# Performance work log

Measured on AMD Instinct MI355X. Metric: run time of the kernel, lower is better.

## Reference

```python
import math
import jax, jax.numpy as jnp
import numpy as np

L, D, DFF, V, TCTX, H = 6, 1024, 4096, 32000, 1024, 16
B, T = 2, 1024


def _ln(x, w, b, eps=1e-5):
    mu = jnp.mean(x, axis=-1, keepdims=True)
    var = jnp.var(x, axis=-1, keepdims=True)
    return (x - mu) * jax.lax.rsqrt(var + eps) * w + b


def setup_inputs() -> dict:
    key = jax.random.key(0)
    ks = jax.random.split(key, 8)
    s = 0.02
    s_res = 0.02 / math.sqrt(2 * L)  # out_proj / ffn.2 init
    tok_emb = jax.random.normal(ks[0], (V, D), jnp.float32) * s
    pos_emb = jax.random.normal(ks[1], (TCTX, D), jnp.float32) * s
    qkv_w = jax.random.normal(ks[2], (L, 3 * D, D), jnp.float32) * s
    out_w = jax.random.normal(ks[3], (L, D, D), jnp.float32) * s_res
    ffn1_w = jax.random.normal(ks[4], (L, DFF, D), jnp.float32) * s
    ffn2_w = jax.random.normal(ks[5], (L, D, DFF), jnp.float32) * s_res
    ln1_w = jnp.ones((L, D), jnp.float32); ln1_b = jnp.zeros((L, D), jnp.float32)
    ln2_w = jnp.ones((L, D), jnp.float32); ln2_b = jnp.zeros((L, D), jnp.float32)
    lnf_w = jnp.ones((D,), jnp.float32);  lnf_b = jnp.zeros((D,), jnp.float32)
    idx = jax.random.randint(ks[6], (B, T), 0, V, dtype=jnp.int32)
    return dict(idx=idx, tok_emb=tok_emb, pos_emb=pos_emb,
                ln1_w=ln1_w, ln1_b=ln1_b, qkv_w=qkv_w, out_w=out_w,
                ln2_w=ln2_w, ln2_b=ln2_b, ffn1_w=ffn1_w, ffn2_w=ffn2_w,
                lnf_w=lnf_w, lnf_b=lnf_b)


def reference(idx, tok_emb, pos_emb, ln1_w, ln1_b, qkv_w, out_w,
              ln2_w, ln2_b, ffn1_w, ffn2_w, lnf_w, lnf_b):
    b, t = idx.shape
    d = tok_emb.shape[1]
    hd = d // H
    scale = 1.0 / math.sqrt(hd)
    causal = jnp.tril(jnp.ones((t, t), bool))  # [T,T]

    x = tok_emb[idx] + pos_emb[:t][None]  # [B,T,D]
    n_layers = qkv_w.shape[0]
    for l in range(n_layers):
        # attention
        h = _ln(x, ln1_w[l], ln1_b[l])
        qkv = h @ qkv_w[l].T  # [B,T,3D]
        q, k, v = jnp.split(qkv, 3, axis=-1)
        q = q.reshape(b, t, H, hd); k = k.reshape(b, t, H, hd); v = v.reshape(b, t, H, hd)
        scores = jnp.einsum('bqhd,bkhd->bhqk', q, k) * scale
        scores = jnp.where(causal[None, None], scores, -jnp.inf)
        attn = jax.nn.softmax(scores, axis=-1)
        o = jnp.einsum('bhqk,bkhd->bqhd', attn, v).reshape(b, t, d)
        x = x + o @ out_w[l].T
        # FFN
        h = _ln(x, ln2_w[l], ln2_b[l])
        x = x + jax.nn.gelu(h @ ffn1_w[l].T, approximate=False) @ ffn2_w[l].T
    x = _ln(x, lnf_w, lnf_b)
    logits = x @ tok_emb.T  # tied lm_head, [B,T,V]
    return logits
```

## Files before the change

### kernel.cpp

```cpp
#include <hip/hip_runtime.h>
#include <math.h>

typedef unsigned short u16;
typedef short short8 __attribute__((ext_vector_type(8)));
typedef float floatx4 __attribute__((ext_vector_type(4)));
typedef u16 u16x4 __attribute__((ext_vector_type(4)));

#define L_ 6
#define D_ 1024
#define DFF_ 4096
#define V_ 32000
#define T_ 1024
#define B_ 2
#define H_ 16
#define M_ (B_*T_)

__device__ __forceinline__ float b2f(u16 v){ union{unsigned u; float f;} x; x.u = ((unsigned)v)<<16; return x.f; }
__device__ __forceinline__ u16 f2bf(float f){ union{float f; unsigned u;} x; x.f=f; unsigned r = x.u + 0x7fffu + ((x.u>>16)&1u); return (u16)(r>>16); }

__device__ __forceinline__ void gload16(const u16* g, u16* l){
  __builtin_amdgcn_global_load_lds((const __attribute__((address_space(1))) void*)g,
                                   (__attribute__((address_space(3))) void*)l, 16, 0, 0);
}

__global__ __launch_bounds__(256) void embed_kernel(const int* __restrict__ idx,
    const float* __restrict__ tok, const float* __restrict__ pos, float* __restrict__ x)
{
  int m = blockIdx.x;
  int t = m & (T_-1);
  int id = idx[m];
  int d = threadIdx.x*4;
  floatx4 tv = *(const floatx4*)(tok + (size_t)id*D_ + d);
  floatx4 pv = *(const floatx4*)(pos + (size_t)t*D_ + d);
  floatx4 r = tv + pv;
  *(floatx4*)(x + (size_t)m*D_ + d) = r;
}

__global__ __launch_bounds__(256) void cvt_kernel(const float* __restrict__ src, u16* __restrict__ dst)
{
  size_t i = ((size_t)blockIdx.x*256 + threadIdx.x)*8;
  floatx4 a = *(const floatx4*)(src + i);
  floatx4 b = *(const floatx4*)(src + i + 4);
  short8 o;
  #pragma unroll
  for (int j=0;j<4;j++){ o[j] = (short)f2bf(a[j]); o[4+j] = (short)f2bf(b[j]); }
  *(short8*)(dst + i) = o;
}

__global__ __launch_bounds__(256) void ln_kernel(const float* __restrict__ x,
    const float* __restrict__ w, const float* __restrict__ b, u16* __restrict__ out)
{
  int row = blockIdx.x, tid = threadIdx.x;
  const float* xr = x + (size_t)row*D_;
  floatx4 v = *(const floatx4*)(xr + tid*4);
  float s  = v[0]+v[1]+v[2]+v[3];
  float sq = v[0]*v[0]+v[1]*v[1]+v[2]*v[2]+v[3]*v[3];
  #pragma unroll
  for (int m=32;m>0;m>>=1){ s += __shfl_xor(s,m); sq += __shfl_xor(sq,m); }
  __shared__ float red[8];
  if ((tid&63)==0){ red[tid>>6]=s; red[4+(tid>>6)]=sq; }
  __syncthreads();
  float st  = red[0]+red[1]+red[2]+red[3];
  float sqt = red[4]+red[5]+red[6]+red[7];
  float mu = st*(1.0f/D_);
  float rs = rsqrtf(sqt*(1.0f/D_) - mu*mu + 1e-5f);
  floatx4 wv = *(const floatx4*)(w + tid*4);
  floatx4 bv = *(const floatx4*)(b + tid*4);
  u16x4 o;
  #pragma unroll
  for(int j=0;j<4;j++) o[j] = f2bf((v[j]-mu)*rs*wv[j] + bv[j]);
  *(u16x4*)(out + (size_t)row*D_ + tid*4) = o;
}

#define BM 128
#define BN 128
#define BK 32

__global__ __launch_bounds__(256) void gemm_bf16(const u16* __restrict__ A,
    const u16* __restrict__ Bw, void* __restrict__ Cp,
    int M, int N, int K, int mode, int gy)
{
  __shared__ __align__(16) u16 As[2*BM*BK];
  __shared__ __align__(16) u16 Bs[2*BN*BK];
  int tid = threadIdx.x;

  int bid = blockIdx.x, nwg = gridDim.x;
  int xcd = bid & 7, o8 = bid >> 3;
  int q = nwg >> 3, r = nwg & 7;
  int wg = (xcd < r ? xcd*(q+1) : r*(q+1) + (xcd-r)*q) + o8;
  int n0 = (wg / gy) * BN;
  int m0 = (wg % gy) * BM;

  int w = tid>>6, lane = tid&63, quad = lane>>4, r16 = lane&15;
  int wm = (w>>1)*64, wn = (w&1)*64;

  int c0 = w*128 + lane;
  int c1 = c0 + 64;
  const u16* ga0 = A  + (size_t)(m0 + (c0>>2))*K + (c0&3)*8;
  const u16* ga1 = A  + (size_t)(m0 + (c1>>2))*K + (c1&3)*8;
  const u16* gb0 = Bw + (size_t)(n0 + (c0>>2))*K + (c0&3)*8;
  const u16* gb1 = Bw + (size_t)(n0 + (c1>>2))*K + (c1&3)*8;

  floatx4 acc[4][4];
  #pragma unroll
  for(int i=0;i<4;i++)
    #pragma unroll
    for(int j=0;j<4;j++) acc[i][j] = (floatx4)0.0f;

  int nt = K/BK;
  gload16(ga0, As + w*1024);
  gload16(ga1, As + w*1024 + 512);
  gload16(gb0, Bs + w*1024);
  gload16(gb1, Bs + w*1024 + 512);
  __syncthreads();

  int cur = 0;
  for (int t=0; t<nt; ++t){
    if (t+1 < nt){
      int kn = (t+1)*BK;
      int nb = (cur^1)*(BM*BK);
      gload16(ga0 + kn, As + nb + w*1024);
      gload16(ga1 + kn, As + nb + w*1024 + 512);
      gload16(gb0 + kn, Bs + nb + w*1024);
      gload16(gb1 + kn, Bs + nb + w*1024 + 512);
    }
    const u16* Ab = As + cur*(BM*BK);
    const u16* Bb = Bs + cur*(BN*BK);
    short8 af[4], bfr[4];
    #pragma unroll
    for (int i=0;i<4;i++){
      af[i]  = *(const short8*)(Ab + (wm + i*16 + r16)*BK + quad*8);
      bfr[i] = *(const short8*)(Bb + (wn + i*16 + r16)*BK + quad*8);
    }
    #pragma unroll
    for (int mi=0;mi<4;mi++)
      #pragma unroll
      for (int ni=0;ni<4;ni++)
        acc[mi][ni] = __builtin_amdgcn_mfma_f32_16x16x32_bf16(af[mi], bfr[ni], acc[mi][ni], 0,0,0);
    __syncthreads();
    cur ^= 1;
  }

  #pragma unroll
  for (int mi=0;mi<4;mi++){
    #pragma unroll
    for (int ni=0;ni<4;ni++){
      #pragma unroll
      for (int r2=0;r2<4;r2++){
        int m = m0 + wm + mi*16 + quad*4 + r2;
        int n = n0 + wn + ni*16 + r16;
        float v = acc[mi][ni][r2];
        size_t off = (size_t)m*N + n;
        if (mode==1)      ((float*)Cp)[off] = v;
        else if (mode==2) ((u16*)Cp)[off]   = f2bf(0.5f*v*(1.0f + erff(v*0.70710678118654752f)));
        else if (mode==4) ((u16*)Cp)[off]   = f2bf(v);
        else              ((float*)Cp)[off] += v;
      }
    }
  }
}

__global__ __launch_bounds__(256) void vtrans_kernel(const u16* __restrict__ qkv, u16* __restrict__ Vt)
{
  __shared__ u16 Lt[64*72];
  int bh = blockIdx.x, b = bh>>4, h = bh&15;
  int tt = blockIdx.y;
  int tid = threadIdx.x;
  #pragma unroll
  for (int cc=0; cc<2; cc++){
    int c = tid + cc*256;
    int t = c>>3, dc = (c&7)*8;
    short8 v = *(const short8*)(qkv + ((size_t)(b*T_) + tt*64 + t)*3072 + 2048 + h*64 + dc);
    *(short8*)(Lt + t*72 + dc) = v;
  }
  __syncthreads();
  #pragma unroll
  for (int cc=0; cc<2; cc++){
    int c = tid + cc*256;
    int d = c>>3, tc = (c&7)*8;
    short8 o;
    #pragma unroll
    for (int j=0;j<8;j++) o[j] = (short)Lt[(tc+j)*72 + d];
    *(short8*)(Vt + ((size_t)bh*64 + d)*T_ + tt*64 + tc) = o;
  }
}

__global__ __launch_bounds__(256) void attn_mfma(const u16* __restrict__ qkv,
    const u16* __restrict__ Vt, u16* __restrict__ out)
{
  __shared__ __align__(16) u16 Qs[64*72];
  __shared__ __align__(16) u16 Ksh[64*72];
  __shared__ __align__(16) u16 Vts[64*72];
  __shared__ __align__(16) u16 Pls[4][16*72];
  int bh = blockIdx.x, b = bh>>4, h = bh&15;
  int y = blockIdx.y;
  int qt = (y<8) ? y : 23-y;
  int tid = threadIdx.x, w = tid>>6, lane = tid&63, quad = lane>>4, r16 = lane&15;

  #pragma unroll
  for (int cc=0; cc<2; cc++){
    int c = tid + cc*256;
    int r = c>>3, dc = (c&7)*8;
    short8 v = *(const short8*)(qkv + ((size_t)(b*T_) + qt*64 + r)*3072 + h*64 + dc);
    *(short8*)(Qs + r*72 + dc) = v;
  }
  __syncthreads();
  short8 qf[2];
  qf[0] = *(const short8*)(Qs + (w*16 + r16)*72 + quad*8);
  qf[1] = *(const short8*)(Qs + (w*16 + r16)*72 + quad*8 + 32);

  floatx4 oacc[4];
  #pragma unroll
  for (int i=0;i<4;i++) oacc[i] = (floatx4)0.0f;
  float m_run[4], l_run[4];
  #pragma unroll
  for (int r=0;r<4;r++){ m_run[r] = -INFINITY; l_run[r] = 0.f; }
  int qg = qt*64 + w*16 + quad*4;

  for (int kb=0; kb<=qt; kb++){
    __syncthreads();
    #pragma unroll
    for (int cc=0; cc<2; cc++){
      int c = tid + cc*256;
      int r = c>>3, dc = (c&7)*8;
      short8 kv = *(const short8*)(qkv + ((size_t)(b*T_) + kb*64 + r)*3072 + D_ + h*64 + dc);
      *(short8*)(Ksh + r*72 + dc) = kv;
      short8 vv = *(const short8*)(Vt + ((size_t)bh*64 + r)*T_ + kb*64 + dc);
      *(short8*)(Vts + r*72 + dc) = vv;
    }
    __syncthreads();

    floatx4 sa[4];
    #pragma unroll
    for (int nt=0;nt<4;nt++) sa[nt] = (floatx4)0.0f;
    #pragma unroll
    for (int nt=0;nt<4;nt++){
      short8 kf0 = *(const short8*)(Ksh + (nt*16 + r16)*72 + quad*8);
      short8 kf1 = *(const short8*)(Ksh + (nt*16 + r16)*72 + quad*8 + 32);
      sa[nt] = __builtin_amdgcn_mfma_f32_16x16x32_bf16(qf[0], kf0, sa[nt], 0,0,0);
      sa[nt] = __builtin_amdgcn_mfma_f32_16x16x32_bf16(qf[1], kf1, sa[nt], 0,0,0);
    }
    bool diag = (kb==qt);
    #pragma unroll
    for (int nt=0;nt<4;nt++)
      #pragma unroll
      for (int r=0;r<4;r++){
        float s = sa[nt][r]*0.125f;
        if (diag && (kb*64 + nt*16 + r16) > (qg + r)) s = -INFINITY;
        sa[nt][r] = s;
      }

    float mt[4];
    #pragma unroll
    for (int r=0;r<4;r++) mt[r] = fmaxf(fmaxf(sa[0][r],sa[1][r]), fmaxf(sa[2][r],sa[3][r]));
    #pragma unroll
    for (int msk=1; msk<16; msk<<=1)
      #pragma unroll
      for (int r=0;r<4;r++) mt[r] = fmaxf(mt[r], __shfl_xor(mt[r], msk));
    float alpha[4];
    #pragma unroll
    for (int r=0;r<4;r++){
      float nm = fmaxf(m_run[r], mt[r]);
      alpha[r] = __expf(m_run[r]-nm);
      m_run[r] = nm;
    }
    float psum[4] = {0.f,0.f,0.f,0.f};
    #pragma unroll
    for (int nt=0;nt<4;nt++)
      #pragma unroll
      for (int r=0;r<4;r++){
        float p = __expf(sa[nt][r]-m_run[r]);
        sa[nt][r] = p;
        psum[r] += p;
      }
    #pragma unroll
    for (int msk=1; msk<16; msk<<=1)
      #pragma unroll
      for (int r=0;r<4;r++) psum[r] += __shfl_xor(psum[r], msk);
    #pragma unroll
    for (int r=0;r<4;r++) l_run[r] = l_run[r]*alpha[r] + psum[r];
    #pragma unroll
    for (int nt=0;nt<4;nt++)
      #pragma unroll
      for (int r=0;r<4;r++) oacc[nt][r] *= alpha[r];

    #pragma unroll
    for (int nt=0;nt<4;nt++)
      #pragma unroll
      for (int r=0;r<4;r++)
        Pls[w][(quad*4+r)*72 + nt*16 + r16] = f2bf(sa[nt][r]);
    short8 pf0 = *(const short8*)(&Pls[w][r16*72 + quad*8]);
    short8 pf1 = *(const short8*)(&Pls[w][r16*72 + quad*8 + 32]);

    #pragma unroll
    for (int nt=0;nt<4;nt++){
      short8 vf0 = *(const short8*)(Vts + (nt*16 + r16)*72 + quad*8);
      short8 vf1 = *(const short8*)(Vts + (nt*16 + r16)*72 + quad*8 + 32);
      oacc[nt] = __builtin_amdgcn_mfma_f32_16x16x32_bf16(pf0, vf0, oacc[nt], 0,0,0);
      oacc[nt] = __builtin_amdgcn_mfma_f32_16x16x32_bf16(pf1, vf1, oacc[nt], 0,0,0);
    }
  }

  float inv[4];
  #pragma unroll
  for (int r=0;r<4;r++) inv[r] = 1.f/l_run[r];
  #pragma unroll
  for (int nt=0;nt<4;nt++)
    #pragma unroll
    for (int r=0;r<4;r++)
      out[((size_t)(b*T_) + qt*64 + w*16 + quad*4 + r)*D_ + h*64 + nt*16 + r16] = f2bf(oacc[nt][r]*inv[r]);
}

extern "C" void kernel_launch(void* const* d_in, const int* in_sizes, int n_in,
                              void* d_out, int out_size, void* d_ws, size_t ws_size,
                              hipStream_t stream)
{
  const int*   idx = (const int*)d_in[0];
  const float* tok = (const float*)d_in[1];
  const float* pos = (const float*)d_in[2];
  const float* ln1w = (const float*)d_in[3];
  const float* ln1b = (const float*)d_in[4];
  const float* qkvw = (const float*)d_in[5];
  const float* outw = (const float*)d_in[6];
  const float* ln2w = (const float*)d_in[7];
  const float* ln2b = (const float*)d_in[8];
  const float* f1w  = (const float*)d_in[9];
  const float* f2w  = (const float*)d_in[10];
  const float* lnfw = (const float*)d_in[11];
  const float* lnfb = (const float*)d_in[12];

  char* ws = (char*)d_ws;
  float* x   = (float*)ws;
  u16*  h    = (u16*) (ws + (size_t)( 8<<20));
  u16*  qkv  = (u16*) (ws + (size_t)(12<<20));
  u16*  ao   = (u16*) (ws + (size_t)(24<<20));
  u16*  ff   = (u16*) (ws + (size_t)(28<<20));
  u16*  vt   = (u16*) (ws + (size_t)(44<<20));
  u16*  wb   = (u16*) (ws + (size_t)(48<<20));
  if (ws_size < ((size_t)120<<20)) return;

  const int GY = M_/BM;
  embed_kernel<<<M_, 256, 0, stream>>>(idx, tok, pos, x);
  for (int l=0; l<L_; l++){
    ln_kernel<<<M_, 256, 0, stream>>>(x, ln1w + l*D_, ln1b + l*D_, h);
    cvt_kernel<<<(3*D_*D_)/2048, 256, 0, stream>>>(qkvw + (size_t)l*3*D_*D_, wb);
    gemm_bf16<<<(3*D_/BN)*GY, 256, 0, stream>>>(h, wb, qkv, M_, 3*D_, D_, 4, GY);
    vtrans_kernel<<<dim3(B_*H_, T_/64), 256, 0, stream>>>(qkv, vt);
    attn_mfma<<<dim3(B_*H_, T_/64), 256, 0, stream>>>(qkv, vt, ao);
    cvt_kernel<<<(D_*D_)/2048, 256, 0, stream>>>(outw + (size_t)l*D_*D_, wb);
    gemm_bf16<<<(D_/BN)*GY, 256, 0, stream>>>(ao, wb, x, M_, D_, D_, 3, GY);
    ln_kernel<<<M_, 256, 0, stream>>>(x, ln2w + l*D_, ln2b + l*D_, h);
    cvt_kernel<<<(DFF_*D_)/2048, 256, 0, stream>>>(f1w + (size_t)l*DFF_*D_, wb);
    gemm_bf16<<<(DFF_/BN)*GY, 256, 0, stream>>>(h, wb, ff, M_, DFF_, D_, 2, GY);
    cvt_kernel<<<(D_*DFF_)/2048, 256, 0, stream>>>(f2w + (size_t)l*D_*DFF_, wb);
    gemm_bf16<<<(D_/BN)*GY, 256, 0, stream>>>(ff, wb, x, M_, D_, DFF_, 3, GY);
  }
  ln_kernel<<<M_, 256, 0, stream>>>(x, lnfw, lnfb, h);
  cvt_kernel<<<(V_*D_)/2048, 256, 0, stream>>>(tok, wb);
  gemm_bf16<<<(V_/BN)*GY, 256, 0, stream>>>(h, wb, (float*)d_out, M_, V_, D_, 1, GY);
}
```

Baseline: 2.348 ms.

## Add split-K with atomic accumulation for residual GEMMs and swizzle LDS tiles

```diff
diff --git a/kernel.cpp b/kernel.cpp
--- a/kernel.cpp
+++ b/kernel.cpp
@@ -78,7 +78,7 @@
 
 __global__ __launch_bounds__(256) void gemm_bf16(const u16* __restrict__ A,
     const u16* __restrict__ Bw, void* __restrict__ Cp,
-    int M, int N, int K, int mode, int gy)
+    int M, int N, int K, int mode, int gy, int sk)
 {
   __shared__ __align__(16) u16 As[2*BM*BK];
   __shared__ __align__(16) u16 Bs[2*BN*BK];
@@ -88,18 +88,26 @@
   int xcd = bid & 7, o8 = bid >> 3;
   int q = nwg >> 3, r = nwg & 7;
   int wg = (xcd < r ? xcd*(q+1) : r*(q+1) + (xcd-r)*q) + o8;
-  int n0 = (wg / gy) * BN;
-  int m0 = (wg % gy) * BM;
+  int body = nwg / sk;
+  int s    = wg / body;
+  int rem  = wg % body;
+  int n0 = (rem / gy) * BN;
+  int m0 = (rem % gy) * BM;
+  int Ks   = K / sk;
+  int kb0  = s * Ks;
 
   int w = tid>>6, lane = tid&63, quad = lane>>4, r16 = lane&15;
   int wm = (w>>1)*64, wn = (w&1)*64;
 
   int c0 = w*128 + lane;
   int c1 = c0 + 64;
-  const u16* ga0 = A  + (size_t)(m0 + (c0>>2))*K + (c0&3)*8;
-  const u16* ga1 = A  + (size_t)(m0 + (c1>>2))*K + (c1&3)*8;
-  const u16* gb0 = Bw + (size_t)(n0 + (c0>>2))*K + (c0&3)*8;
-  const u16* gb1 = Bw + (size_t)(n0 + (c1>>2))*K + (c1&3)*8;
+  int r0 = c0>>2, r1 = c1>>2;
+  int sg0 = (c0&3) ^ ((r0>>1)&3);
+  int sg1 = (c1&3) ^ ((r1>>1)&3);
+  const u16* ga0 = A  + (size_t)(m0 + r0)*K + kb0 + sg0*8;
+  const u16* ga1 = A  + (size_t)(m0 + r1)*K + kb0 + sg1*8;
+  const u16* gb0 = Bw + (size_t)(n0 + r0)*K + kb0 + sg0*8;
+  const u16* gb1 = Bw + (size_t)(n0 + r1)*K + kb0 + sg1*8;
 
   floatx4 acc[4][4];
   #pragma unroll
@@ -107,16 +115,17 @@
     #pragma unroll
     for(int j=0;j<4;j++) acc[i][j] = (floatx4)0.0f;
 
-  int nt = K/BK;
+  int ntk = Ks/BK;
   gload16(ga0, As + w*1024);
   gload16(ga1, As + w*1024 + 512);
   gload16(gb0, Bs + w*1024);
   gload16(gb1, Bs + w*1024 + 512);
   __syncthreads();
 
+  int sl = (quad ^ ((r16>>1)&3))*8;
   int cur = 0;
-  for (int t=0; t<nt; ++t){
-    if (t+1 < nt){
+  for (int t=0; t<ntk; ++t){
+    if (t+1 < ntk){
       int kn = (t+1)*BK;
       int nb = (cur^1)*(BM*BK);
       gload16(ga0 + kn, As + nb + w*1024);
@@ -129,8 +138,8 @@
     short8 af[4], bfr[4];
     #pragma unroll
     for (int i=0;i<4;i++){
-      af[i]  = *(const short8*)(Ab + (wm + i*16 + r16)*BK + quad*8);
-      bfr[i] = *(const short8*)(Bb + (wn + i*16 + r16)*BK + quad*8);
+      af[i]  = *(const short8*)(Ab + (wm + i*16 + r16)*BK + sl);
+      bfr[i] = *(const short8*)(Bb + (wn + i*16 + r16)*BK + sl);
     }
     #pragma unroll
     for (int mi=0;mi<4;mi++)
@@ -154,7 +163,7 @@
         if (mode==1)      ((float*)Cp)[off] = v;
         else if (mode==2) ((u16*)Cp)[off]   = f2bf(0.5f*v*(1.0f + erff(v*0.70710678118654752f)));
         else if (mode==4) ((u16*)Cp)[off]   = f2bf(v);
-        else              ((float*)Cp)[off] += v;
+        else              atomicAdd((float*)Cp + off, v);
       }
     }
   }
@@ -344,18 +353,18 @@
   for (int l=0; l<L_; l++){
     ln_kernel<<<M_, 256, 0, stream>>>(x, ln1w + l*D_, ln1b + l*D_, h);
     cvt_kernel<<<(3*D_*D_)/2048, 256, 0, stream>>>(qkvw + (size_t)l*3*D_*D_, wb);
-    gemm_bf16<<<(3*D_/BN)*GY, 256, 0, stream>>>(h, wb, qkv, M_, 3*D_, D_, 4, GY);
+    gemm_bf16<<<(3*D_/BN)*GY, 256, 0, stream>>>(h, wb, qkv, M_, 3*D_, D_, 4, GY, 1);
     vtrans_kernel<<<dim3(B_*H_, T_/64), 256, 0, stream>>>(qkv, vt);
     attn_mfma<<<dim3(B_*H_, T_/64), 256, 0, stream>>>(qkv, vt, ao);
     cvt_kernel<<<(D_*D_)/2048, 256, 0, stream>>>(outw + (size_t)l*D_*D_, wb);
-    gemm_bf16<<<(D_/BN)*GY, 256, 0, stream>>>(ao, wb, x, M_, D_, D_, 3, GY);
+    gemm_bf16<<<(D_/BN)*GY*2, 256, 0, stream>>>(ao, wb, x, M_, D_, D_, 3, GY, 2);
     ln_kernel<<<M_, 256, 0, stream>>>(x, ln2w + l*D_, ln2b + l*D_, h);
     cvt_kernel<<<(DFF_*D_)/2048, 256, 0, stream>>>(f1w + (size_t)l*DFF_*D_, wb);
-    gemm_bf16<<<(DFF_/BN)*GY, 256, 0, stream>>>(h, wb, ff, M_, DFF_, D_, 2, GY);
+    gemm_bf16<<<(DFF_/BN)*GY, 256, 0, stream>>>(h, wb, ff, M_, DFF_, D_, 2, GY, 1);
     cvt_kernel<<<(D_*DFF_)/2048, 256, 0, stream>>>(f2w + (size_t)l*D_*DFF_, wb);
-    gemm_bf16<<<(D_/BN)*GY, 256, 0, stream>>>(ff, wb, x, M_, D_, DFF_, 3, GY);
+    gemm_bf16<<<(D_/BN)*GY*4, 256, 0, stream>>>(ff, wb, x, M_, D_, DFF_, 3, GY, 4);
   }
   ln_kernel<<<M_, 256, 0, stream>>>(x, lnfw, lnfb, h);
   cvt_kernel<<<(V_*D_)/2048, 256, 0, stream>>>(tok, wb);
-  gemm_bf16<<<(V_/BN)*GY, 256, 0, stream>>>(h, wb, (float*)d_out, M_, V_, D_, 1, GY);
-}
+  gemm_bf16<<<(V_/BN)*GY, 256, 0, stream>>>(h, wb, (float*)d_out, M_, V_, D_, 1, GY, 1);
+}
```

Result: faster. 1.978 ms (-15.8%).
